# Kernel optimization log

Measured on AMD Instinct MI355X. Metric: run time of the kernel, lower is better.

Reference implementation:

```python
import jax, jax.numpy as jnp
import numpy as np

HID = 4

def setup_inputs() -> dict:
    key = jax.random.key(0)
    ks = jax.random.split(key, 8)
    B, T, F = 4096, 512, 16
    x = jax.random.normal(ks[0], (B, T, F), dtype=jnp.float32)
    # Keras LSTMCell params: kernel [F,4H], recurrent_kernel [H,4H], bias [4H] (gate order i,f,c,o)
    Wk = jax.random.normal(ks[1], (F, 4 * HID), dtype=jnp.float32) * 0.1
    Wr = jax.random.normal(ks[2], (HID, 4 * HID), dtype=jnp.float32) * 0.1
    b = jnp.zeros((4 * HID,), dtype=jnp.float32)
    W1 = jax.random.normal(ks[3], (HID, 64), dtype=jnp.float32) * 0.1
    b1 = jnp.zeros((64,), dtype=jnp.float32)
    W2 = jax.random.normal(ks[4], (64, 5), dtype=jnp.float32) * 0.1
    b2 = jnp.zeros((5,), dtype=jnp.float32)
    return {"x": x, "Wk": Wk, "Wr": Wr, "b": b, "W1": W1, "b1": b1, "W2": W2, "b2": b2}

def _lstm_last_h(x, Wk, Wr, b):
    B = x.shape[0]
    # precompute input projections for all timesteps: [T, B, 4H]
    xg = jnp.einsum('btf,fg->tbg', x, Wk) + b

    def step(carry, xg_t):
        h, c = carry
        gates = xg_t + h @ Wr  # [B, 4H]
        i, f, g, o = jnp.split(gates, 4, axis=-1)
        i = jax.nn.sigmoid(i)
        f = jax.nn.sigmoid(f)
        o = jax.nn.sigmoid(o)
        c = f * c + i * jnp.tanh(g)
        h = o * jnp.tanh(c)
        return (h, c), None

    h0 = jnp.zeros((B, HID), dtype=x.dtype)
    c0 = jnp.zeros((B, HID), dtype=x.dtype)
    (h, _), _ = jax.lax.scan(step, (h0, c0), xg)
    return h  # [B, H] -- RNN returns last output only (return_sequences=False)

def reference(x, Wk, Wr, b, W1, b1, W2, b2):
    h = _lstm_last_h(x, Wk, Wr, b)
    h = jax.nn.relu(h @ W1 + b1)
    return jax.nn.softmax(h @ W2 + b2, axis=-1)  # [B, 5]
```

## Files before the change

kernel.cpp:

```cpp
#include <hip/hip_runtime.h>

#define TLEN 512
#define LOG2E 1.44269504088896340736f

#if __has_builtin(__builtin_amdgcn_exp2f)
#define EXP2F(x) __builtin_amdgcn_exp2f(x)
#else
#define EXP2F(x) __exp2f(x)
#endif
#if __has_builtin(__builtin_amdgcn_rcpf)
#define RCPF(x) __builtin_amdgcn_rcpf(x)
#else
#define RCPF(x) (1.0f / (x))
#endif

#define SWZ(v, xm) __int_as_float(__builtin_amdgcn_ds_swizzle(__float_as_int(v), (((xm) << 10) | 0x1F)))
#define DPPF(v, ctrl) __int_as_float(__builtin_amdgcn_update_dpp(__float_as_int(v), __float_as_int(v), (ctrl), 0xF, 0xF, false))
#define QB(v, k) DPPF(v, 0x55 * (k))
#define XOR3(v)  DPPF(v, 0x1B)
#define XOR7(v)  DPPF(v, 0x141)
#define XOR8(v)  DPPF(v, 0x128)

struct X4 { float4 a, b, c, d; };

__global__ __launch_bounds__(256)
__attribute__((amdgpu_waves_per_eu(1, 1)))
void lstm_mlp_kernel(
    const float* __restrict__ x,
    const float* __restrict__ Wk,
    const float* __restrict__ Wr,
    const float* __restrict__ bg,
    const float* __restrict__ W1,
    const float* __restrict__ b1,
    const float* __restrict__ W2,
    const float* __restrict__ b2,
    float* __restrict__ out,
    int B)
{
    const int tid = blockIdx.x * 256 + threadIdx.x;
    const int seq = tid >> 4;
    if (seq >= B) return;
    const int i16 = tid & 15;
    const int j   = i16 >> 2;
    const int q   = i16 & 3;
    const int gate = q * 4 + j;

    const bool is_g = (q == 2);
    const float k1 = is_g ? (-2.0f * LOG2E) : (-LOG2E);
    const float m1c = is_g ? (-4.0f * LOG2E) : 1.0f;
    const float m0c = is_g ? (2.0f * LOG2E) : 0.0f;

    float wk[16];
#pragma unroll
    for (int f = 0; f < 16; ++f) wk[f] = k1 * Wk[f * 16 + gate];
    const float wr0 = k1 * Wr[(j ^ 0) * 16 + gate];
    const float wr1 = k1 * Wr[(j ^ 1) * 16 + gate];
    const float wr2 = k1 * Wr[(j ^ 2) * 16 + gate];
    const float wr3 = k1 * Wr[(j ^ 3) * 16 + gate];
    const float biasS = k1 * bg[gate];

    const X4* xt = reinterpret_cast<const X4*>(x) + (size_t)seq * TLEN;

    float cs = 0.0f, h = 0.0f;

#define DOT4S(v, w0_, w1_, w2_, w3_, seed) \
    fmaf((v).x, (w0_), fmaf((v).y, (w1_), fmaf((v).z, (w2_), fmaf((v).w, (w3_), (seed)))))
#define DOTB(Bk) \
    ((DOT4S((Bk).a, wk[0], wk[1], wk[2], wk[3], biasS) + \
      DOT4S((Bk).b, wk[4], wk[5], wk[6], wk[7], 0.0f)) + \
     (DOT4S((Bk).c, wk[8], wk[9], wk[10], wk[11], 0.0f) + \
      DOT4S((Bk).d, wk[12], wk[13], wk[14], wk[15], 0.0f)))

#define STEP(XD) { \
    float h1_ = XOR7(XOR3(h));    \
    float h2_ = XOR8(h);          \
    float h3_ = XOR8(h1_);        \
    float pre = fmaf(h, wr0, (XD)); \
    pre = fmaf(h2_, wr2, pre); \
    pre = fmaf(h1_, wr1, pre); \
    pre = fmaf(h3_, wr3, pre); \
    float r_ = RCPF(1.0f + EXP2F(pre)); \
    float av = fmaf(m1c, r_, m0c); \
    float iv = QB(av, 0); \
    float fv = QB(av, 1); \
    float gv = QB(av, 2); \
    float ov = QB(av, 3); \
    cs = fmaf(fv, cs, iv * gv); \
    float th_ = fmaf(2.0f, RCPF(1.0f + EXP2F(cs)), -1.0f); \
    h = ov * th_; }

    X4 B0 = xt[0], B1 = xt[1], B2 = xt[2], B3 = xt[3];
    X4 B4 = xt[4], B5 = xt[5], B6 = xt[6], B7 = xt[7];

    for (int t = 0; t < TLEN - 8; t += 8) {
        { float xd = DOTB(B0); B0 = xt[t +  8]; STEP(xd); }
        { float xd = DOTB(B1); B1 = xt[t +  9]; STEP(xd); }
        { float xd = DOTB(B2); B2 = xt[t + 10]; STEP(xd); }
        { float xd = DOTB(B3); B3 = xt[t + 11]; STEP(xd); }
        { float xd = DOTB(B4); B4 = xt[t + 12]; STEP(xd); }
        { float xd = DOTB(B5); B5 = xt[t + 13]; STEP(xd); }
        { float xd = DOTB(B6); B6 = xt[t + 14]; STEP(xd); }
        { float xd = DOTB(B7); B7 = xt[t + 15]; STEP(xd); }
    }
    { float xd = DOTB(B0); STEP(xd); }
    { float xd = DOTB(B1); STEP(xd); }
    { float xd = DOTB(B2); STEP(xd); }
    { float xd = DOTB(B3); STEP(xd); }
    { float xd = DOTB(B4); STEP(xd); }
    { float xd = DOTB(B5); STEP(xd); }
    { float xd = DOTB(B6); STEP(xd); }
    { float xd = DOTB(B7); STEP(xd); }

    float hA = h;
    float hB = SWZ(h, 4), hC = SWZ(h, 8), hD = SWZ(h, 12);

    float p0 = 0.f, p1 = 0.f, p2 = 0.f, p3 = 0.f, p4 = 0.f;
#pragma unroll
    for (int r = 0; r < 4; ++r) {
        const int u = i16 * 4 + r;
        float acc = b1[u];
        acc = fmaf(hA, W1[(j ^ 0) * 64 + u], acc);
        acc = fmaf(hB, W1[(j ^ 1) * 64 + u], acc);
        acc = fmaf(hC, W1[(j ^ 2) * 64 + u], acc);
        acc = fmaf(hD, W1[(j ^ 3) * 64 + u], acc);
        acc = fmaxf(acc, 0.0f);
        p0 = fmaf(acc, W2[u * 5 + 0], p0);
        p1 = fmaf(acc, W2[u * 5 + 1], p1);
        p2 = fmaf(acc, W2[u * 5 + 2], p2);
        p3 = fmaf(acc, W2[u * 5 + 3], p3);
        p4 = fmaf(acc, W2[u * 5 + 4], p4);
    }
    p0 += SWZ(p0, 1); p1 += SWZ(p1, 1); p2 += SWZ(p2, 1); p3 += SWZ(p3, 1); p4 += SWZ(p4, 1);
    p0 += SWZ(p0, 2); p1 += SWZ(p1, 2); p2 += SWZ(p2, 2); p3 += SWZ(p3, 2); p4 += SWZ(p4, 2);
    p0 += SWZ(p0, 4); p1 += SWZ(p1, 4); p2 += SWZ(p2, 4); p3 += SWZ(p3, 4); p4 += SWZ(p4, 4);
    p0 += SWZ(p0, 8); p1 += SWZ(p1, 8); p2 += SWZ(p2, 8); p3 += SWZ(p3, 8); p4 += SWZ(p4, 8);

    p0 += b2[0]; p1 += b2[1]; p2 += b2[2]; p3 += b2[3]; p4 += b2[4];

    float mx = fmaxf(fmaxf(fmaxf(p0, p1), fmaxf(p2, p3)), p4);
    float e0 = EXP2F((p0 - mx) * LOG2E);
    float e1 = EXP2F((p1 - mx) * LOG2E);
    float e2 = EXP2F((p2 - mx) * LOG2E);
    float e3 = EXP2F((p3 - mx) * LOG2E);
    float e4 = EXP2F((p4 - mx) * LOG2E);
    float s = ((e0 + e1) + (e2 + e3)) + e4;
    float rs = RCPF(s);

    if (i16 == 0) {
        float* op = out + (size_t)seq * 5;
        op[0] = e0 * rs; op[1] = e1 * rs; op[2] = e2 * rs;
        op[3] = e3 * rs; op[4] = e4 * rs;
    }
}

extern "C" void kernel_launch(void* const* d_in, const int* in_sizes, int n_in,
                              void* d_out, int out_size, void* d_ws, size_t ws_size,
                              hipStream_t stream) {
    const float* x  = (const float*)d_in[0];
    const float* Wk = (const float*)d_in[1];
    const float* Wr = (const float*)d_in[2];
    const float* bg = (const float*)d_in[3];
    const float* W1 = (const float*)d_in[4];
    const float* b1 = (const float*)d_in[5];
    const float* W2 = (const float*)d_in[6];
    const float* b2 = (const float*)d_in[7];
    float* out = (float*)d_out;

    const int B = in_sizes[0] / (TLEN * 16);
    const int threads = B * 16;
    dim3 block(256);
    dim3 grid((threads + 255) / 256);
    lstm_mlp_kernel<<<grid, block, 0, stream>>>(x, Wk, Wr, bg, W1, b1, W2, b2, out, B);
}
```

Before: 73.45 us.

## Batch input projections into LDS chunks, decoupled from the recurrent loop

Splits the time loop into 32-step chunks. Each thread first computes the input projections for a chunk and stores them in shared memory, then runs the serial recurrence reading those values back from LDS. This takes the global loads and input dot products off the latency-critical recurrent chain, and the recurrent FMA chain is rebalanced into two shorter partial sums. In exchange it adds LDS traffic, drops the sequence bounds check (it now assumes B is a multiple of 16), and loses overlap between loads and the recurrence inside a chunk.

After: 119.0 us. +62.0%, slower.

```diff
diff --git a/kernel.cpp b/kernel.cpp
--- a/kernel.cpp
+++ b/kernel.cpp
@@ -37,13 +37,18 @@
     float* __restrict__ out,
     int B)
 {
-    const int tid = blockIdx.x * 256 + threadIdx.x;
-    const int seq = tid >> 4;
-    if (seq >= B) return;
-    const int i16 = tid & 15;
-    const int j   = i16 >> 2;
-    const int q   = i16 & 3;
+    __shared__ float xg[4][64][36];
+
+    const int tidx = threadIdx.x;
+    const int w    = tidx >> 6;
+    const int sl   = (tidx >> 4) & 3;
+    const int i16  = tidx & 15;
+    const int j    = i16 >> 2;
+    const int q    = i16 & 3;
     const int gate = q * 4 + j;
+    const int row  = sl * 16 + i16;
+
+    const int seq = blockIdx.x * 16 + w * 4 + sl;
 
     const bool is_g = (q == 2);
     const float k1 = is_g ? (-2.0f * LOG2E) : (-LOG2E);
@@ -75,10 +80,9 @@
     float h1_ = XOR7(XOR3(h));    \
     float h2_ = XOR8(h);          \
     float h3_ = XOR8(h1_);        \
-    float pre = fmaf(h, wr0, (XD)); \
-    pre = fmaf(h2_, wr2, pre); \
-    pre = fmaf(h1_, wr1, pre); \
-    pre = fmaf(h3_, wr3, pre); \
+    float preA = fmaf(h, wr0, fmaf(h1_, wr1, (XD))); \
+    float preB = fmaf(h2_, wr2, h3_ * wr3); \
+    float pre = preA + preB; \
     float r_ = RCPF(1.0f + EXP2F(pre)); \
     float av = fmaf(m1c, r_, m0c); \
     float iv = QB(av, 0); \
@@ -89,27 +93,37 @@
     float th_ = fmaf(2.0f, RCPF(1.0f + EXP2F(cs)), -1.0f); \
     h = ov * th_; }
 
-    X4 B0 = xt[0], B1 = xt[1], B2 = xt[2], B3 = xt[3];
-    X4 B4 = xt[4], B5 = xt[5], B6 = xt[6], B7 = xt[7];
+    float* const xrow = &xg[w][row][0];
 
-    for (int t = 0; t < TLEN - 8; t += 8) {
-        { float xd = DOTB(B0); B0 = xt[t +  8]; STEP(xd); }
-        { float xd = DOTB(B1); B1 = xt[t +  9]; STEP(xd); }
-        { float xd = DOTB(B2); B2 = xt[t + 10]; STEP(xd); }
-        { float xd = DOTB(B3); B3 = xt[t + 11]; STEP(xd); }
-        { float xd = DOTB(B4); B4 = xt[t + 12]; STEP(xd); }
-        { float xd = DOTB(B5); B5 = xt[t + 13]; STEP(xd); }
-        { float xd = DOTB(B6); B6 = xt[t + 14]; STEP(xd); }
-        { float xd = DOTB(B7); B7 = xt[t + 15]; STEP(xd); }
+    for (int c = 0; c < 16; ++c) {
+        const int t0 = c * 32;
+
+#pragma unroll 2
+        for (int tt = 0; tt < 32; tt += 4) {
+            X4 v0 = xt[t0 + tt + 0];
+            X4 v1 = xt[t0 + tt + 1];
+            X4 v2 = xt[t0 + tt + 2];
+            X4 v3 = xt[t0 + tt + 3];
+            float4 d;
+            d.x = DOTB(v0);
+            d.y = DOTB(v1);
+            d.z = DOTB(v2);
+            d.w = DOTB(v3);
+            *reinterpret_cast<float4*>(&xrow[tt]) = d;
+        }
+
+        float4 xq = *reinterpret_cast<const float4*>(&xrow[0]);
+#pragma unroll
+        for (int tg = 0; tg < 8; ++tg) {
+            float4 xn;
+            if (tg < 7) xn = *reinterpret_cast<const float4*>(&xrow[(tg + 1) * 4]);
+            STEP(xq.x);
+            STEP(xq.y);
+            STEP(xq.z);
+            STEP(xq.w);
+            if (tg < 7) xq = xn;
+        }
     }
-    { float xd = DOTB(B0); STEP(xd); }
-    { float xd = DOTB(B1); STEP(xd); }
-    { float xd = DOTB(B2); STEP(xd); }
-    { float xd = DOTB(B3); STEP(xd); }
-    { float xd = DOTB(B4); STEP(xd); }
-    { float xd = DOTB(B5); STEP(xd); }
-    { float xd = DOTB(B6); STEP(xd); }
-    { float xd = DOTB(B7); STEP(xd); }
 
     float hA = h;
     float hB = SWZ(h, 4), hC = SWZ(h, 8), hD = SWZ(h, 12);
@@ -167,8 +181,7 @@
     float* out = (float*)d_out;
 
     const int B = in_sizes[0] / (TLEN * 16);
-    const int threads = B * 16;
     dim3 block(256);
-    dim3 grid((threads + 255) / 256);
+    dim3 grid(B / 16);
     lstm_mlp_kernel<<<grid, block, 0, stream>>>(x, Wk, Wr, bg, W1, b1, W2, b2, out, B);
 }
```

## Split input projection across two half-lane groups and pipeline it ahead of recurrence

Applied to the files above, without the earlier changes.

Each sequence now uses 32 lanes instead of 16. Each half computes an 8-feature partial dot product of the input projection, and the halves are combined with a swizzle, so each thread holds half as much x data. The projections are computed four steps ahead in a rotating queue so the input FMAs stay off the recurrent critical path, and the recurrent FMA chain is split into two shorter partial sums. Occupancy is raised to two waves per EU. The cost is twice as many threads doing the recurrent step redundantly, plus an extra cross-lane swizzle per step.

Measured after the change: 112.4 us. +53.0%, slower.

```diff
diff --git a/kernel.cpp b/kernel.cpp
--- a/kernel.cpp
+++ b/kernel.cpp
@@ -15,16 +15,17 @@
 #endif
 
 #define SWZ(v, xm) __int_as_float(__builtin_amdgcn_ds_swizzle(__float_as_int(v), (((xm) << 10) | 0x1F)))
+#define SWZ16(v)   __int_as_float(__builtin_amdgcn_ds_swizzle(__float_as_int(v), 0x401F))
 #define DPPF(v, ctrl) __int_as_float(__builtin_amdgcn_update_dpp(__float_as_int(v), __float_as_int(v), (ctrl), 0xF, 0xF, false))
 #define QB(v, k) DPPF(v, 0x55 * (k))
 #define XOR3(v)  DPPF(v, 0x1B)
 #define XOR7(v)  DPPF(v, 0x141)
 #define XOR8(v)  DPPF(v, 0x128)
 
-struct X4 { float4 a, b, c, d; };
+struct XH { float4 a, b; };
 
 __global__ __launch_bounds__(256)
-__attribute__((amdgpu_waves_per_eu(1, 1)))
+__attribute__((amdgpu_waves_per_eu(2, 2)))
 void lstm_mlp_kernel(
     const float* __restrict__ x,
     const float* __restrict__ Wk,
@@ -37,12 +38,12 @@
     float* __restrict__ out,
     int B)
 {
-    const int tid = blockIdx.x * 256 + threadIdx.x;
-    const int seq = tid >> 4;
-    if (seq >= B) return;
-    const int i16 = tid & 15;
-    const int j   = i16 >> 2;
-    const int q   = i16 & 3;
+    const int tid  = blockIdx.x * 256 + threadIdx.x;
+    const int seq  = tid >> 5;
+    const int half = (tid >> 4) & 1;
+    const int i16  = tid & 15;
+    const int j    = i16 >> 2;
+    const int q    = i16 & 3;
     const int gate = q * 4 + j;
 
     const bool is_g = (q == 2);
@@ -50,35 +51,34 @@
     const float m1c = is_g ? (-4.0f * LOG2E) : 1.0f;
     const float m0c = is_g ? (2.0f * LOG2E) : 0.0f;
 
-    float wk[16];
+    float wk[8];
 #pragma unroll
-    for (int f = 0; f < 16; ++f) wk[f] = k1 * Wk[f * 16 + gate];
+    for (int f = 0; f < 8; ++f) wk[f] = k1 * Wk[(half * 8 + f) * 16 + gate];
     const float wr0 = k1 * Wr[(j ^ 0) * 16 + gate];
     const float wr1 = k1 * Wr[(j ^ 1) * 16 + gate];
     const float wr2 = k1 * Wr[(j ^ 2) * 16 + gate];
     const float wr3 = k1 * Wr[(j ^ 3) * 16 + gate];
-    const float biasS = k1 * bg[gate];
+    const float biasS = (half == 0) ? (k1 * bg[gate]) : 0.0f;
 
-    const X4* xt = reinterpret_cast<const X4*>(x) + (size_t)seq * TLEN;
+    const float4* bp = reinterpret_cast<const float4*>(x + (size_t)seq * TLEN * 16 + half * 8);
 
     float cs = 0.0f, h = 0.0f;
 
 #define DOT4S(v, w0_, w1_, w2_, w3_, seed) \
     fmaf((v).x, (w0_), fmaf((v).y, (w1_), fmaf((v).z, (w2_), fmaf((v).w, (w3_), (seed)))))
-#define DOTB(Bk) \
-    ((DOT4S((Bk).a, wk[0], wk[1], wk[2], wk[3], biasS) + \
-      DOT4S((Bk).b, wk[4], wk[5], wk[6], wk[7], 0.0f)) + \
-     (DOT4S((Bk).c, wk[8], wk[9], wk[10], wk[11], 0.0f) + \
-      DOT4S((Bk).d, wk[12], wk[13], wk[14], wk[15], 0.0f)))
+#define DOT8(S) \
+    (DOT4S((S).a, wk[0], wk[1], wk[2], wk[3], biasS) + \
+     DOT4S((S).b, wk[4], wk[5], wk[6], wk[7], 0.0f))
+#define LOADS(S, T) { S.a = bp[(size_t)(T) * 4]; S.b = bp[(size_t)(T) * 4 + 1]; }
+#define MKXD(S, X) { float pd_ = DOT8(S); X = pd_ + SWZ16(pd_); }
 
 #define STEP(XD) { \
     float h1_ = XOR7(XOR3(h));    \
     float h2_ = XOR8(h);          \
     float h3_ = XOR8(h1_);        \
-    float pre = fmaf(h, wr0, (XD)); \
-    pre = fmaf(h2_, wr2, pre); \
-    pre = fmaf(h1_, wr1, pre); \
-    pre = fmaf(h3_, wr3, pre); \
+    float preA = fmaf(h, wr0, fmaf(h1_, wr1, (XD))); \
+    float preB = fmaf(h2_, wr2, h3_ * wr3); \
+    float pre = preA + preB; \
     float r_ = RCPF(1.0f + EXP2F(pre)); \
     float av = fmaf(m1c, r_, m0c); \
     float iv = QB(av, 0); \
@@ -89,27 +89,37 @@
     float th_ = fmaf(2.0f, RCPF(1.0f + EXP2F(cs)), -1.0f); \
     h = ov * th_; }
 
-    X4 B0 = xt[0], B1 = xt[1], B2 = xt[2], B3 = xt[3];
-    X4 B4 = xt[4], B5 = xt[5], B6 = xt[6], B7 = xt[7];
+#define BODY(S, TN) { \
+    STEP(X0); X0 = X1; X1 = X2; X2 = X3; \
+    MKXD(S, X3); \
+    LOADS(S, TN); }
 
-    for (int t = 0; t < TLEN - 8; t += 8) {
-        { float xd = DOTB(B0); B0 = xt[t +  8]; STEP(xd); }
-        { float xd = DOTB(B1); B1 = xt[t +  9]; STEP(xd); }
-        { float xd = DOTB(B2); B2 = xt[t + 10]; STEP(xd); }
-        { float xd = DOTB(B3); B3 = xt[t + 11]; STEP(xd); }
-        { float xd = DOTB(B4); B4 = xt[t + 12]; STEP(xd); }
-        { float xd = DOTB(B5); B5 = xt[t + 13]; STEP(xd); }
-        { float xd = DOTB(B6); B6 = xt[t + 14]; STEP(xd); }
-        { float xd = DOTB(B7); B7 = xt[t + 15]; STEP(xd); }
+#define MIN511(a) ((a) > 511 ? 511 : (a))
+
+    XH S0, S1, S2, S3, S4, S5, S6, S7;
+    LOADS(S0, 0); LOADS(S1, 1); LOADS(S2, 2); LOADS(S3, 3);
+    LOADS(S4, 4); LOADS(S5, 5); LOADS(S6, 6); LOADS(S7, 7);
+
+    float X0, X1, X2, X3;
+    MKXD(S0, X0); MKXD(S1, X1); MKXD(S2, X2); MKXD(S3, X3);
+
+#pragma clang loop unroll(disable)
+    for (int t = 0; t < 504; t += 8) {
+        const int tn = t + 12;
+        BODY(S4, MIN511(tn));
+        BODY(S5, MIN511(tn + 1));
+        BODY(S6, MIN511(tn + 2));
+        BODY(S7, MIN511(tn + 3));
+        BODY(S0, MIN511(tn + 4));
+        BODY(S1, MIN511(tn + 5));
+        BODY(S2, MIN511(tn + 6));
+        BODY(S3, MIN511(tn + 7));
     }
-    { float xd = DOTB(B0); STEP(xd); }
-    { float xd = DOTB(B1); STEP(xd); }
-    { float xd = DOTB(B2); STEP(xd); }
-    { float xd = DOTB(B3); STEP(xd); }
-    { float xd = DOTB(B4); STEP(xd); }
-    { float xd = DOTB(B5); STEP(xd); }
-    { float xd = DOTB(B6); STEP(xd); }
-    { float xd = DOTB(B7); STEP(xd); }
+    { STEP(X0); X0 = X1; X1 = X2; X2 = X3; MKXD(S4, X3); }
+    { STEP(X0); X0 = X1; X1 = X2; X2 = X3; MKXD(S5, X3); }
+    { STEP(X0); X0 = X1; X1 = X2; X2 = X3; MKXD(S6, X3); }
+    { STEP(X0); X0 = X1; X1 = X2; X2 = X3; MKXD(S7, X3); }
+    STEP(X0); STEP(X1); STEP(X2); STEP(X3);
 
     float hA = h;
     float hB = SWZ(h, 4), hC = SWZ(h, 8), hD = SWZ(h, 12);
@@ -146,7 +156,7 @@
     float s = ((e0 + e1) + (e2 + e3)) + e4;
     float rs = RCPF(s);
 
-    if (i16 == 0) {
+    if ((tid & 31) == 0) {
         float* op = out + (size_t)seq * 5;
         op[0] = e0 * rs; op[1] = e1 * rs; op[2] = e2 * rs;
         op[3] = e3 * rs; op[4] = e4 * rs;
@@ -167,7 +177,7 @@
     float* out = (float*)d_out;
 
     const int B = in_sizes[0] / (TLEN * 16);
-    const int threads = B * 16;
+    const int threads = B * 32;
     dim3 block(256);
     dim3 grid((threads + 255) / 256);
     lstm_mlp_kernel<<<grid, block, 0, stream>>>(x, Wk, Wr, bg, W1, b1, W2, b2, out, B);
```

## Batch input projections per 32-step chunk and split recurrent dot into two chains

Applied to the files above, without the earlier changes.

The time loop becomes 16 chunks of 32 steps. Each chunk first loads x and computes all 32 input projections, then a scheduling barrier separates that from the serial recurrent steps. The intent is to take memory loads and input FMAs off the latency-bound recurrence. The recurrent preactivation is also split into two independent FMA chains to shorten the dependency chain. The cost is that loads are no longer overlapped with the recurrence, so each chunk waits on memory before it can start, and register pressure goes up.

Measured after the change: 99.36 us. 35.3% more time.

```diff
diff --git a/kernel.cpp b/kernel.cpp
--- a/kernel.cpp
+++ b/kernel.cpp
@@ -75,10 +75,9 @@
     float h1_ = XOR7(XOR3(h));    \
     float h2_ = XOR8(h);          \
     float h3_ = XOR8(h1_);        \
-    float pre = fmaf(h, wr0, (XD)); \
-    pre = fmaf(h2_, wr2, pre); \
-    pre = fmaf(h1_, wr1, pre); \
-    pre = fmaf(h3_, wr3, pre); \
+    float preA = fmaf(h, wr0, fmaf(h1_, wr1, (XD))); \
+    float preB = fmaf(h2_, wr2, h3_ * wr3); \
+    float pre = preA + preB; \
     float r_ = RCPF(1.0f + EXP2F(pre)); \
     float av = fmaf(m1c, r_, m0c); \
     float iv = QB(av, 0); \
@@ -89,27 +88,24 @@
     float th_ = fmaf(2.0f, RCPF(1.0f + EXP2F(cs)), -1.0f); \
     h = ov * th_; }
 
-    X4 B0 = xt[0], B1 = xt[1], B2 = xt[2], B3 = xt[3];
-    X4 B4 = xt[4], B5 = xt[5], B6 = xt[6], B7 = xt[7];
+#pragma clang loop unroll(disable)
+    for (int c = 0; c < 16; ++c) {
+        const X4* xc = xt + c * 32;
+        float xd[32];
 
-    for (int t = 0; t < TLEN - 8; t += 8) {
-        { float xd = DOTB(B0); B0 = xt[t +  8]; STEP(xd); }
-        { float xd = DOTB(B1); B1 = xt[t +  9]; STEP(xd); }
-        { float xd = DOTB(B2); B2 = xt[t + 10]; STEP(xd); }
-        { float xd = DOTB(B3); B3 = xt[t + 11]; STEP(xd); }
-        { float xd = DOTB(B4); B4 = xt[t + 12]; STEP(xd); }
-        { float xd = DOTB(B5); B5 = xt[t + 13]; STEP(xd); }
-        { float xd = DOTB(B6); B6 = xt[t + 14]; STEP(xd); }
-        { float xd = DOTB(B7); B7 = xt[t + 15]; STEP(xd); }
+#pragma unroll
+        for (int t = 0; t < 32; ++t) {
+            X4 v = xc[t];
+            xd[t] = DOTB(v);
+        }
+
+        __builtin_amdgcn_sched_barrier(0);
+
+#pragma unroll
+        for (int t = 0; t < 32; ++t) {
+            STEP(xd[t]);
+        }
     }
-    { float xd = DOTB(B0); STEP(xd); }
-    { float xd = DOTB(B1); STEP(xd); }
-    { float xd = DOTB(B2); STEP(xd); }
-    { float xd = DOTB(B3); STEP(xd); }
-    { float xd = DOTB(B4); STEP(xd); }
-    { float xd = DOTB(B5); STEP(xd); }
-    { float xd = DOTB(B6); STEP(xd); }
-    { float xd = DOTB(B7); STEP(xd); }
 
     float hA = h;
     float hB = SWZ(h, 4), hC = SWZ(h, 8), hD = SWZ(h, 12);
```
